# Optimization experiments

Hardware: AMD Instinct MI355X
Metric: run time of the kernel (lower is better)

The kernel has to match this reference:

```python
import jax, jax.numpy as jnp
import numpy as np

EPS = 1e-12  # F.normalize eps
TEMP = 0.03


def _l2norm(x):
    # torch F.normalize: x / max(||x||, eps)
    n = jnp.sqrt(jnp.sum(x * x, axis=-1, keepdims=True))
    return x / jnp.maximum(n, EPS)


def setup_inputs() -> dict:
    key = jax.random.key(0)
    ks = jax.random.split(key, 8)
    B, C, H, W = 8, 256, 64, 64
    M = 2024
    Ch = C // 4
    s = 1.0 / np.sqrt(C)
    return {
        "feats": jax.random.normal(ks[0], (B, C, H, W), jnp.float32),
        "fg_memory": jax.random.normal(ks[1], (M, C), jnp.float32) * s,
        "bg_memory": jax.random.normal(ks[2], (M, C), jnp.float32) * s,
        "w1_fg": jax.random.normal(ks[3], (C, Ch), jnp.float32) * s,
        "b1_fg": jnp.zeros((Ch,), jnp.float32),
        "w2_fg": jax.random.normal(ks[4], (Ch, 1), jnp.float32) * (1.0 / np.sqrt(Ch)),
        "b2_fg": jnp.zeros((1,), jnp.float32),
        "w1_bg": jax.random.normal(ks[5], (C, Ch), jnp.float32) * s,
        "b1_bg": jnp.zeros((Ch,), jnp.float32),
        "w2_bg": jax.random.normal(ks[6], (Ch, 1), jnp.float32) * (1.0 / np.sqrt(Ch)),
        "b2_bg": jnp.zeros((1,), jnp.float32),
    }


def _gate(x, w1, b1, w2, b2):
    h = jax.nn.relu(x @ w1 + b1)
    return jax.nn.sigmoid(h @ w2 + b2)  # [N,1]


def reference(feats, fg_memory, bg_memory, w1_fg, b1_fg, w2_fg, b2_fg,
              w1_bg, b1_bg, w2_bg, b2_bg):
    B, C, H, W = feats.shape
    x = jnp.transpose(feats, (0, 2, 3, 1)).reshape(-1, C)  # [N,C]
    xn = _l2norm(x)
    fgn = _l2norm(fg_memory)  # [M,C]
    bgn = _l2norm(bg_memory)

    attn_fg = jax.nn.softmax((xn @ fgn.T) / TEMP, axis=1)  # [N,M]
    mem_fg = attn_fg @ fgn                                  # [N,C]
    attn_bg = jax.nn.softmax((xn @ bgn.T) / TEMP, axis=1)
    mem_bg = attn_bg @ bgn

    g_fg = _gate(xn, w1_fg, b1_fg, w2_fg, b2_fg)
    g_bg = _gate(xn, w1_bg, b1_bg, w2_bg, b2_bg)

    fused = xn + g_fg * mem_fg - g_bg * mem_bg
    return jnp.transpose(fused.reshape(B, H, W, C), (0, 3, 1, 2))
```

## Files before the change

### kernel.cpp

```cpp
#include <hip/hip_runtime.h>
#include <math.h>

#define B_   8
#define C_   256
#define HW_  4096
#define N_   32768
#define M_   2024
#define MP_  2048
#define CH_  64
#define NCHUNK (MP_ / 64)
#define INV_TEMP 33.333333333333336f
#define NEPS 1e-12f

typedef __attribute__((ext_vector_type(8))) short short8;
typedef __attribute__((ext_vector_type(4))) float floatx4;

__device__ __forceinline__ float wred64(float s) {
#pragma unroll
  for (int off = 32; off > 0; off >>= 1) s += __shfl_xor(s, off, 64);
  return s;
}

__device__ __forceinline__ unsigned short f2bf(float f) {
  union { float f; unsigned u; } v; v.f = f;
  unsigned r = v.u + 0x7FFFu + ((v.u >> 16) & 1u);
  return (unsigned short)(r >> 16);
}
__device__ __forceinline__ float bf2f(unsigned short b) {
  union { unsigned u; float f; } v; v.u = ((unsigned)b) << 16; return v.f;
}

__device__ __forceinline__ void barrier_lds_only() {
  asm volatile("s_waitcnt lgkmcnt(0)\n\ts_barrier" ::: "memory");
}

__device__ __forceinline__ void async_copy16(const unsigned short* gsrc,
                                             unsigned short* lds) {
  __builtin_amdgcn_global_load_lds(
      (const __attribute__((address_space(1))) void*)gsrc,
      (__attribute__((address_space(3))) void*)lds, 16, 0, 0);
}

__global__ __launch_bounds__(256) void norm_mem_kernel(
    const float* __restrict__ fg, const float* __restrict__ bg,
    unsigned short* __restrict__ fgS, unsigned short* __restrict__ bgS,
    unsigned short* __restrict__ fgT, unsigned short* __restrict__ bgT) {
  __shared__ unsigned short tile[64][258];
  int bid = blockIdx.x;
  const float* src; unsigned short *ms, *mt; int r0;
  if (bid < 32) { src = fg; ms = fgS; mt = fgT; r0 = bid * 64; }
  else          { src = bg; ms = bgS; mt = bgT; r0 = (bid - 32) * 64; }
  int t = threadIdx.x;
  int rr = t >> 2, c4 = t & 3;
  int row = r0 + rr;
  int chunk = r0 >> 6;
  float v[64];
  float s = 0.f;
  if (row < M_) {
    const float4* p = (const float4*)(src + (size_t)row * C_ + c4 * 64);
#pragma unroll
    for (int i = 0; i < 16; ++i) {
      float4 q = p[i];
      v[i * 4 + 0] = q.x; v[i * 4 + 1] = q.y; v[i * 4 + 2] = q.z; v[i * 4 + 3] = q.w;
      s += q.x * q.x + q.y * q.y + q.z * q.z + q.w * q.w;
    }
  } else {
#pragma unroll
    for (int i = 0; i < 64; ++i) v[i] = 0.f;
  }
  s += __shfl_xor(s, 1, 64);
  s += __shfl_xor(s, 2, 64);
  float inv = (row < M_) ? 1.0f / fmaxf(sqrtf(s), NEPS) : 0.f;
#pragma unroll
  for (int i = 0; i < 16; ++i) {
    int c = c4 * 64 + i * 4;
    ushort4 o;
    o.x = f2bf(v[i * 4 + 0] * inv); o.y = f2bf(v[i * 4 + 1] * inv);
    o.z = f2bf(v[i * 4 + 2] * inv); o.w = f2bf(v[i * 4 + 3] * inv);
    int unit = (chunk * 32 + (c >> 5) * 4 + ((c >> 3) & 3)) * 64 + rr;
    *(ushort4*)&ms[(size_t)unit * 8 + (c & 7)] = o;
    *(ushort4*)&tile[rr][c] = o;
  }
  __syncthreads();
  int m = t & 63, cw = t >> 6;
#pragma unroll 8
  for (int j = 0; j < 64; ++j) {
    int c = cw * 64 + j;
    mt[(size_t)c * MP_ + r0 + m] = tile[m][c];
  }
}

__global__ __launch_bounds__(256) void prep_x_kernel(
    const float* __restrict__ feats, float* __restrict__ invn,
    unsigned short* __restrict__ xnb) {
  __shared__ unsigned short tileb[256][66];
  __shared__ float part[4][64];
  __shared__ float invs[64];
  int t = threadIdx.x, hwl = t & 63, cw = t >> 6;
  int n0 = blockIdx.x * 64;
  int b = n0 >> 12, hw0 = n0 & 4095;
  const float* p = feats + (size_t)b * C_ * HW_ + hw0 + hwl;
  float s = 0.f;
#pragma unroll 8
  for (int i = 0; i < 64; ++i) {
    int c = cw * 64 + i;
    float v = p[(size_t)c * HW_];
    s += v * v;
    tileb[c][hwl] = f2bf(v);
  }
  part[cw][hwl] = s;
  __syncthreads();
  if (t < 64) {
    float tot = part[0][t] + part[1][t] + part[2][t] + part[3][t];
    float inv = 1.0f / fmaxf(sqrtf(tot), NEPS);
    invn[n0 + t] = inv;
    invs[t] = inv;
  }
  __syncthreads();
  int px = t >> 2, q = t & 3;
  float iv = invs[px];
  unsigned short* xp = xnb + (size_t)(n0 + px) * C_;
#pragma unroll
  for (int blk = 0; blk < 8; ++blk) {
    int cb = blk * 4 + q;
    short8 o;
#pragma unroll
    for (int j = 0; j < 8; ++j)
      o[j] = (short)f2bf(bf2f(tileb[cb * 8 + j][px]) * iv);
    *(short8*)&xp[cb * 8] = o;
  }
}

__global__ __launch_bounds__(256) void gate_kernel(
    const unsigned short* __restrict__ xnb,
    const float* __restrict__ w1f, const float* __restrict__ b1f,
    const float* __restrict__ w2f, const float* __restrict__ b2f,
    const float* __restrict__ w1b, const float* __restrict__ b1b,
    const float* __restrict__ w2b, const float* __restrict__ b2b,
    float* __restrict__ gf, float* __restrict__ gb) {
  __shared__ float xr[16][C_];
  int t = threadIdx.x, w = t >> 6, lane = t & 63;
  int n0 = blockIdx.x * 16;
#pragma unroll
  for (int pp = 0; pp < 4; ++pp) {
    int px = w * 4 + pp;
    ushort4 u = *(const ushort4*)&xnb[(size_t)(n0 + px) * C_ + lane * 4];
    xr[px][lane * 4 + 0] = bf2f(u.x);
    xr[px][lane * 4 + 1] = bf2f(u.y);
    xr[px][lane * 4 + 2] = bf2f(u.z);
    xr[px][lane * 4 + 3] = bf2f(u.w);
  }
  __syncthreads();
  float hf[4], hb[4];
#pragma unroll
  for (int pp = 0; pp < 4; ++pp) { hf[pp] = b1f[lane]; hb[pp] = b1b[lane]; }
#pragma unroll 4
  for (int c = 0; c < C_; ++c) {
    float wf = w1f[c * CH_ + lane];
    float wb = w1b[c * CH_ + lane];
#pragma unroll
    for (int pp = 0; pp < 4; ++pp) {
      float x = xr[w * 4 + pp][c];
      hf[pp] += x * wf;
      hb[pp] += x * wb;
    }
  }
  float b2fv = b2f[0], b2bv = b2b[0];
#pragma unroll
  for (int pp = 0; pp < 4; ++pp) {
    float sf = fmaxf(hf[pp], 0.f) * w2f[lane];
    float sb = fmaxf(hb[pp], 0.f) * w2b[lane];
    sf = wred64(sf);
    sb = wred64(sb);
    if (lane == 0) {
      gf[n0 + w * 4 + pp] = 1.f / (1.f + __expf(-(sf + b2fv)));
      gb[n0 + w * 4 + pp] = 1.f / (1.f + __expf(-(sb + b2bv)));
    }
  }
}

__device__ __forceinline__ void stage_chunk(const unsigned short* memS, int mc,
                                            unsigned short* mtile, int w, int l) {
  const unsigned short* src = memS + (size_t)mc * 16384;
#pragma unroll
  for (int it = 0; it < 4; ++it) {
    int seg = (it * 8 + w) * 512;
    async_copy16(src + seg + l * 8, mtile + seg);
  }
}

__global__ __launch_bounds__(512, 4) void flash_fused_kernel(
    const unsigned short* __restrict__ xnb,
    const unsigned short* __restrict__ fgS, const unsigned short* __restrict__ fgT,
    const unsigned short* __restrict__ bgS, const unsigned short* __restrict__ bgT,
    const float* __restrict__ gf, const float* __restrict__ gb,
    const float* __restrict__ feats, const float* __restrict__ invn,
    float* __restrict__ out) {
  __shared__ __align__(16) char smem[49664];
  unsigned short* mtile = (unsigned short*)smem;
  unsigned short* Pbuf0 = (unsigned short*)(smem + 32768);
  unsigned short* Pbuf1 = (unsigned short*)(smem + 40960);
  float* rowsum = (float*)(smem + 49152);
  float* comb   = (float*)(smem + 49408);
  float* trans  = (float*)smem;

  int t = threadIdx.x;
  int w = t >> 6, l = t & 63;
  int lm = l & 15, quad = l >> 4;
  int rg = w & 3, mh = w >> 2;
  int row0 = blockIdx.x * 64;

  short8 afrag[8];
  {
    const unsigned short* ap = xnb + (size_t)(row0 + 16 * rg + lm) * C_ + quad * 8;
#pragma unroll
    for (int kb = 0; kb < 8; ++kb)
      afrag[kb] = *(const short8*)(ap + kb * 32);
  }

  int bb = row0 >> 12, hw0 = row0 & 4095;
  float iv = invn[row0 + l];
  size_t ob = (size_t)bb * (size_t)C_ * HW_ + hw0 + l;

#pragma unroll 1
  for (int pass = 0; pass < 2; ++pass) {
    const unsigned short* memS  = pass ? bgS : fgS;
    const unsigned short* membT = pass ? bgT : fgT;
    const float* gp = pass ? gb : gf;

    floatx4 accO[4][2];
#pragma unroll
    for (int rt = 0; rt < 4; ++rt)
#pragma unroll
      for (int ct = 0; ct < 2; ++ct) accO[rt][ct] = (floatx4){0.f, 0.f, 0.f, 0.f};
    float rs[4] = {0.f, 0.f, 0.f, 0.f};
    if (t < 64) rowsum[t] = 0.f;

    stage_chunk(memS, 0, mtile, w, l);

#pragma unroll 1
    for (int mc = 0; mc < NCHUNK; ++mc) {
      __syncthreads();

      short8 bfT[2][2];
#pragma unroll
      for (int ct = 0; ct < 2; ++ct) {
        const unsigned short* tp =
            membT + (size_t)(w * 32 + ct * 16 + lm) * MP_ + mc * 64 + quad * 8;
        bfT[ct][0] = *(const short8*)(tp);
        bfT[ct][1] = *(const short8*)(tp + 32);
      }

      floatx4 accS[2];
      accS[0] = (floatx4){0.f, 0.f, 0.f, 0.f};
      accS[1] = (floatx4){0.f, 0.f, 0.f, 0.f};
#pragma unroll
      for (int mt2 = 0; mt2 < 2; ++mt2) {
        int mrow = mh * 32 + mt2 * 16 + lm;
#pragma unroll
        for (int kb = 0; kb < 8; ++kb) {
          short8 bf = *(const short8*)&mtile[(size_t)(((kb * 4 + quad) * 64) + mrow) * 8];
          accS[mt2] = __builtin_amdgcn_mfma_f32_16x16x32_bf16(afrag[kb], bf, accS[mt2], 0, 0, 0);
        }
      }

      unsigned short* P = (mc & 1) ? Pbuf1 : Pbuf0;
#pragma unroll
      for (int mt2 = 0; mt2 < 2; ++mt2) {
        int m = mh * 32 + mt2 * 16 + lm;
        bool valid = (mc * 64 + m < M_);
        int g = mh * 4 + mt2 * 2 + (lm >> 3);
#pragma unroll
        for (int r = 0; r < 4; ++r) {
          float pv = valid ? __expf(accS[mt2][r] * INV_TEMP) : 0.f;
          unsigned short pb = f2bf(pv);
          rs[r] += bf2f(pb);
          P[(g * 64 + 16 * rg + quad * 4 + r) * 8 + (lm & 7)] = pb;
        }
      }
      barrier_lds_only();

      if (mc + 1 < NCHUNK) stage_chunk(memS, mc + 1, mtile, w, l);

#pragma unroll
      for (int rt = 0; rt < 4; ++rt) {
        short8 pf0 = *(const short8*)&P[(size_t)((0 + quad) * 64 + rt * 16 + lm) * 8];
        short8 pf1 = *(const short8*)&P[(size_t)((4 + quad) * 64 + rt * 16 + lm) * 8];
#pragma unroll
        for (int ct = 0; ct < 2; ++ct) {
          accO[rt][ct] = __builtin_amdgcn_mfma_f32_16x16x32_bf16(pf0, bfT[ct][0], accO[rt][ct], 0, 0, 0);
          accO[rt][ct] = __builtin_amdgcn_mfma_f32_16x16x32_bf16(pf1, bfT[ct][1], accO[rt][ct], 0, 0, 0);
        }
      }
    }

#pragma unroll
    for (int off = 1; off < 16; off <<= 1)
#pragma unroll
      for (int r = 0; r < 4; ++r) rs[r] += __shfl_xor(rs[r], off, 64);
    if (lm == 0) {
#pragma unroll
      for (int r = 0; r < 4; ++r) atomicAdd(&rowsum[16 * rg + quad * 4 + r], rs[r]);
    }
    __syncthreads();
    if (t < 64) comb[t] = gp[row0 + t] / rowsum[t];
    __syncthreads();

#pragma unroll 1
    for (int cg2 = 0; cg2 < 4; ++cg2) {
      if ((w >> 1) == cg2) {
#pragma unroll
        for (int rt = 0; rt < 4; ++rt)
#pragma unroll
          for (int r = 0; r < 4; ++r) {
            float cf = comb[16 * rt + quad * 4 + r];
#pragma unroll
            for (int ct = 0; ct < 2; ++ct)
              trans[(16 * rt + quad * 4 + r) * 67 + (w & 1) * 32 + ct * 16 + lm] =
                  cf * accO[rt][ct][r];
          }
      }
      __syncthreads();
      if (pass == 0) {
#pragma unroll
        for (int i = 0; i < 8; ++i) {
          int cl = w * 8 + i;
          int cg = cg2 * 64 + cl;
          out[ob + (size_t)cg * HW_] = trans[l * 67 + cl];
        }
      } else {
#pragma unroll
        for (int i = 0; i < 8; ++i) {
          int cl = w * 8 + i;
          int cg = cg2 * 64 + cl;
          size_t a = ob + (size_t)cg * HW_;
          out[a] = feats[a] * iv + out[a] - trans[l * 67 + cl];
        }
      }
      __syncthreads();
    }
  }
}

extern "C" void kernel_launch(void* const* d_in, const int* in_sizes, int n_in,
                              void* d_out, int out_size, void* d_ws, size_t ws_size,
                              hipStream_t stream) {
  const float* feats = (const float*)d_in[0];
  const float* fg    = (const float*)d_in[1];
  const float* bg    = (const float*)d_in[2];
  const float* w1f   = (const float*)d_in[3];
  const float* b1f   = (const float*)d_in[4];
  const float* w2f   = (const float*)d_in[5];
  const float* b2f   = (const float*)d_in[6];
  const float* w1b   = (const float*)d_in[7];
  const float* b1b   = (const float*)d_in[8];
  const float* w2b   = (const float*)d_in[9];
  const float* b2b   = (const float*)d_in[10];
  float* out = (float*)d_out;

  char* ws = (char*)d_ws;
  unsigned short* xnb = (unsigned short*)ws;
  unsigned short* fgS = xnb + (size_t)N_ * C_;
  unsigned short* bgS = fgS + (size_t)MP_ * C_;
  unsigned short* fgT = bgS + (size_t)MP_ * C_;
  unsigned short* bgT = fgT + (size_t)C_ * MP_;
  float* gf   = (float*)(bgT + (size_t)C_ * MP_);
  float* gb   = gf + N_;
  float* invn = gb + N_;

  norm_mem_kernel<<<64, 256, 0, stream>>>(fg, bg, fgS, bgS, fgT, bgT);
  prep_x_kernel<<<N_ / 64, 256, 0, stream>>>(feats, invn, xnb);
  gate_kernel<<<N_ / 16, 256, 0, stream>>>(xnb, w1f, b1f, w2f, b2f,
                                           w1b, b1b, w2b, b2b, gf, gb);
  flash_fused_kernel<<<N_ / 64, 512, 0, stream>>>(
      xnb, fgS, fgT, bgS, bgT, gf, gb, feats, invn, out);
}
```

Baseline: 359.9 us.

## Remap score MFMA so each B fragment feeds two row tiles, single P buffer

Warps in the score phase now own a 16-wide memory slice and two 16-row activation tiles, so each LDS B-fragment load feeds two MFMAs instead of one. The P buffer is single-buffered, which frees shared memory. Invalid padded columns are masked with an additive bias inside the exp instead of a branch. s_setprio hints are placed around the MFMA sections. In exchange the kernel holds twice as many A fragments in registers, and the single P buffer relies on the existing barriers being placed correctly to avoid reuse hazards.

New measurement: 541.5 us. 1.5x slower.

```diff
diff --git a/kernel.cpp b/kernel.cpp
--- a/kernel.cpp
+++ b/kernel.cpp
@@ -196,31 +196,32 @@
     const float* __restrict__ gf, const float* __restrict__ gb,
     const float* __restrict__ feats, const float* __restrict__ invn,
     float* __restrict__ out) {
-  __shared__ __align__(16) char smem[49664];
+  __shared__ __align__(16) char smem[41472];
   unsigned short* mtile = (unsigned short*)smem;
-  unsigned short* Pbuf0 = (unsigned short*)(smem + 32768);
-  unsigned short* Pbuf1 = (unsigned short*)(smem + 40960);
-  float* rowsum = (float*)(smem + 49152);
-  float* comb   = (float*)(smem + 49408);
+  unsigned short* Pbuf  = (unsigned short*)(smem + 32768);
+  float* rowsum = (float*)(smem + 40960);
+  float* comb   = (float*)(smem + 41216);
   float* trans  = (float*)smem;
 
   int t = threadIdx.x;
   int w = t >> 6, l = t & 63;
   int lm = l & 15, quad = l >> 4;
-  int rg = w & 3, mh = w >> 2;
+  int mq = w & 3, ph = w >> 2;
   int row0 = blockIdx.x * 64;
 
-  short8 afrag[8];
+  short8 afrag[2][8];
   {
-    const unsigned short* ap = xnb + (size_t)(row0 + 16 * rg + lm) * C_ + quad * 8;
-#pragma unroll
-    for (int kb = 0; kb < 8; ++kb)
-      afrag[kb] = *(const short8*)(ap + kb * 32);
-  }
-
-  int bb = row0 >> 12, hw0 = row0 & 4095;
-  float iv = invn[row0 + l];
-  size_t ob = (size_t)bb * (size_t)C_ * HW_ + hw0 + l;
+    const unsigned short* ap = xnb + (size_t)(row0 + ph * 32 + lm) * C_ + quad * 8;
+#pragma unroll
+    for (int at = 0; at < 2; ++at)
+#pragma unroll
+      for (int kb = 0; kb < 8; ++kb)
+        afrag[at][kb] = *(const short8*)(ap + at * 16 * C_ + kb * 32);
+  }
+
+  int mb = (quad * 64 + mq * 16 + lm) * 8;
+  int wb = ((mq * 2 + (lm >> 3)) * 64 + ph * 32 + quad * 4) * 8 + (lm & 7);
+  int rb = (quad * 64 + lm) * 8;
 
 #pragma unroll 1
   for (int pass = 0; pass < 2; ++pass) {
@@ -233,7 +234,11 @@
     for (int rt = 0; rt < 4; ++rt)
 #pragma unroll
       for (int ct = 0; ct < 2; ++ct) accO[rt][ct] = (floatx4){0.f, 0.f, 0.f, 0.f};
-    float rs[4] = {0.f, 0.f, 0.f, 0.f};
+    float rs[2][4];
+#pragma unroll
+    for (int at = 0; at < 2; ++at)
+#pragma unroll
+      for (int r = 0; r < 4; ++r) rs[at][r] = 0.f;
     if (t < 64) rowsum[t] = 0.f;
 
     stage_chunk(memS, 0, mtile, w, l);
@@ -241,6 +246,31 @@
 #pragma unroll 1
     for (int mc = 0; mc < NCHUNK; ++mc) {
       __syncthreads();
+
+      float ebias = (mc * 64 + mq * 16 + lm < M_) ? 0.f : -1e30f;
+
+      floatx4 accS[2];
+      accS[0] = (floatx4){0.f, 0.f, 0.f, 0.f};
+      accS[1] = (floatx4){0.f, 0.f, 0.f, 0.f};
+      __builtin_amdgcn_s_setprio(1);
+#pragma unroll
+      for (int kb = 0; kb < 8; ++kb) {
+        short8 bf = *(const short8*)&mtile[mb + kb * 2048];
+        accS[0] = __builtin_amdgcn_mfma_f32_16x16x32_bf16(afrag[0][kb], bf, accS[0], 0, 0, 0);
+        accS[1] = __builtin_amdgcn_mfma_f32_16x16x32_bf16(afrag[1][kb], bf, accS[1], 0, 0, 0);
+      }
+      __builtin_amdgcn_s_setprio(0);
+
+#pragma unroll
+      for (int at = 0; at < 2; ++at) {
+#pragma unroll
+        for (int r = 0; r < 4; ++r) {
+          float pv = __expf(__builtin_fmaf(accS[at][r], INV_TEMP, ebias));
+          unsigned short pb = f2bf(pv);
+          rs[at][r] += bf2f(pb);
+          Pbuf[wb + at * 128 + r * 8] = pb;
+        }
+      }
 
       short8 bfT[2][2];
 #pragma unroll
@@ -251,61 +281,43 @@
         bfT[ct][1] = *(const short8*)(tp + 32);
       }
 
-      floatx4 accS[2];
-      accS[0] = (floatx4){0.f, 0.f, 0.f, 0.f};
-      accS[1] = (floatx4){0.f, 0.f, 0.f, 0.f};
-#pragma unroll
-      for (int mt2 = 0; mt2 < 2; ++mt2) {
-        int mrow = mh * 32 + mt2 * 16 + lm;
-#pragma unroll
-        for (int kb = 0; kb < 8; ++kb) {
-          short8 bf = *(const short8*)&mtile[(size_t)(((kb * 4 + quad) * 64) + mrow) * 8];
-          accS[mt2] = __builtin_amdgcn_mfma_f32_16x16x32_bf16(afrag[kb], bf, accS[mt2], 0, 0, 0);
-        }
-      }
-
-      unsigned short* P = (mc & 1) ? Pbuf1 : Pbuf0;
-#pragma unroll
-      for (int mt2 = 0; mt2 < 2; ++mt2) {
-        int m = mh * 32 + mt2 * 16 + lm;
-        bool valid = (mc * 64 + m < M_);
-        int g = mh * 4 + mt2 * 2 + (lm >> 3);
-#pragma unroll
-        for (int r = 0; r < 4; ++r) {
-          float pv = valid ? __expf(accS[mt2][r] * INV_TEMP) : 0.f;
-          unsigned short pb = f2bf(pv);
-          rs[r] += bf2f(pb);
-          P[(g * 64 + 16 * rg + quad * 4 + r) * 8 + (lm & 7)] = pb;
-        }
-      }
       barrier_lds_only();
 
       if (mc + 1 < NCHUNK) stage_chunk(memS, mc + 1, mtile, w, l);
 
+      __builtin_amdgcn_s_setprio(1);
 #pragma unroll
       for (int rt = 0; rt < 4; ++rt) {
-        short8 pf0 = *(const short8*)&P[(size_t)((0 + quad) * 64 + rt * 16 + lm) * 8];
-        short8 pf1 = *(const short8*)&P[(size_t)((4 + quad) * 64 + rt * 16 + lm) * 8];
-#pragma unroll
-        for (int ct = 0; ct < 2; ++ct) {
-          accO[rt][ct] = __builtin_amdgcn_mfma_f32_16x16x32_bf16(pf0, bfT[ct][0], accO[rt][ct], 0, 0, 0);
-          accO[rt][ct] = __builtin_amdgcn_mfma_f32_16x16x32_bf16(pf1, bfT[ct][1], accO[rt][ct], 0, 0, 0);
-        }
-      }
+        short8 pf0 = *(const short8*)&Pbuf[rb + rt * 128];
+        accO[rt][0] = __builtin_amdgcn_mfma_f32_16x16x32_bf16(pf0, bfT[0][0], accO[rt][0], 0, 0, 0);
+        accO[rt][1] = __builtin_amdgcn_mfma_f32_16x16x32_bf16(pf0, bfT[1][0], accO[rt][1], 0, 0, 0);
+        short8 pf1 = *(const short8*)&Pbuf[rb + rt * 128 + 2048];
+        accO[rt][0] = __builtin_amdgcn_mfma_f32_16x16x32_bf16(pf1, bfT[0][1], accO[rt][0], 0, 0, 0);
+        accO[rt][1] = __builtin_amdgcn_mfma_f32_16x16x32_bf16(pf1, bfT[1][1], accO[rt][1], 0, 0, 0);
+      }
+      __builtin_amdgcn_s_setprio(0);
     }
 
 #pragma unroll
     for (int off = 1; off < 16; off <<= 1)
 #pragma unroll
-      for (int r = 0; r < 4; ++r) rs[r] += __shfl_xor(rs[r], off, 64);
+      for (int at = 0; at < 2; ++at)
+#pragma unroll
+        for (int r = 0; r < 4; ++r) rs[at][r] += __shfl_xor(rs[at][r], off, 64);
     if (lm == 0) {
 #pragma unroll
-      for (int r = 0; r < 4; ++r) atomicAdd(&rowsum[16 * rg + quad * 4 + r], rs[r]);
+      for (int at = 0; at < 2; ++at)
+#pragma unroll
+        for (int r = 0; r < 4; ++r)
+          atomicAdd(&rowsum[ph * 32 + at * 16 + quad * 4 + r], rs[at][r]);
     }
     __syncthreads();
     if (t < 64) comb[t] = gp[row0 + t] / rowsum[t];
     __syncthreads();
 
+    float iv = invn[row0 + l];
+    int bb = row0 >> 12, hw0 = row0 & 4095;
+    size_t ob = (size_t)bb * (size_t)C_ * HW_ + hw0 + l;
 #pragma unroll 1
     for (int cg2 = 0; cg2 < 4; ++cg2) {
       if ((w >> 1) == cg2) {
```
